# Performance work log

Measured on AMD Instinct MI355X. Metric: run time of the kernel, lower is better.

## Reference

```python
import jax, jax.numpy as jnp
import numpy as np

B, D, U1, U2 = 16384, 512, 512, 512
BN_EPS = 1e-3  # keras BatchNormalization default epsilon


def sparsemax(z):
    # z: [..., D]; standard sparsemax along last axis (Martins & Astudillo)
    d = z.shape[-1]
    z_sorted = -jnp.sort(-z, axis=-1)                      # descending
    z_cum = jnp.cumsum(z_sorted, axis=-1)
    k = jnp.arange(1, d + 1, dtype=z.dtype)
    support = (1.0 + k * z_sorted) > z_cum                 # [..., D] bool
    k_z = jnp.sum(support, axis=-1, keepdims=True)         # support size
    tau = (jnp.take_along_axis(z_cum, k_z.astype(jnp.int32) - 1, axis=-1) - 1.0) / k_z.astype(z.dtype)
    return jnp.maximum(z - tau, 0.0)


def setup_inputs() -> dict:
    key = jax.random.key(0)
    ks = jax.random.split(key, 8)
    x = jax.random.normal(ks[0], (B, D), dtype=jnp.float32)
    W1 = jax.random.normal(ks[1], (D, U1), dtype=jnp.float32) * 0.05
    b1 = jnp.zeros((U1,), jnp.float32)
    centers = jax.random.normal(ks[2], (U2, D), dtype=jnp.float32)      # paraboloid centers
    coefs = jax.random.normal(ks[3], (U2, D), dtype=jnp.float32) * 0.1  # paraboloid axis coefficients
    bn_gamma = jnp.ones((D,), jnp.float32)
    bn_beta = jnp.zeros((D,), jnp.float32)
    bn_mean = jnp.zeros((D,), jnp.float32)
    bn_var = jnp.ones((D,), jnp.float32)
    W_out = jax.random.normal(ks[4], (U1 + U2, D), dtype=jnp.float32) * 0.05
    b_out = jnp.zeros((D,), jnp.float32)
    w_add = jnp.array([0.5, 0.5], jnp.float32)  # WeightedAdd learnable scalars
    return {"x": x, "W1": W1, "b1": b1, "centers": centers, "coefs": coefs,
            "bn_gamma": bn_gamma, "bn_beta": bn_beta, "bn_mean": bn_mean, "bn_var": bn_var,
            "W_out": W_out, "b_out": b_out, "w_add": w_add}


def reference(x, W1, b1, centers, coefs, bn_gamma, bn_beta, bn_mean, bn_var, W_out, b_out, w_add):
    # Dense branch
    h1 = jax.nn.relu(x @ W1 + b1)                               # [B, U1]
    # BoundedParaboloids branch: BatchNorm (inference stats) then bounded paraboloids
    xb = (x - bn_mean) * jax.lax.rsqrt(bn_var + BN_EPS) * bn_gamma + bn_beta
    # q_j = sum_d (coefs[j,d] * (xb_d - centers[j,d]))^2, computed via GEMMs
    A = coefs * coefs                                            # [U2, D]
    q = (xb * xb) @ A.T - 2.0 * (xb @ (A * centers).T) + jnp.sum(A * centers * centers, axis=-1)
    h2 = jax.nn.relu(1.0 - q)                                    # [B, U2] bounded paraboloids
    # Output embedding: Dense(relu) on concat
    emb = jax.nn.relu(jnp.concatenate([h1, h2], axis=-1) @ W_out + b_out)  # [B, D]
    # WeightedAdd of (dropout-identity) inputs and embedding; dropout_rate=0 / inference
    pre = w_add[0] * x + w_add[1] * emb
    mask = sparsemax(pre)                                        # [B, D]
    return mask
```

## Files before the change

kernel.cpp:

```cpp
#include <hip/hip_runtime.h>
#include <math.h>

typedef float f4 __attribute__((ext_vector_type(4)));
typedef float f32x4 __attribute__((ext_vector_type(4)));
typedef __bf16 bf16x8 __attribute__((ext_vector_type(8)));
typedef unsigned short u16;
typedef u16 us8 __attribute__((ext_vector_type(8)));

__device__ __forceinline__ u16 f2bf(float f) {
  unsigned u = __builtin_bit_cast(unsigned, f);
  unsigned r = u + 0x7fffu + ((u >> 16) & 1u);
  return (u16)(r >> 16);
}
__device__ __forceinline__ float bf2f(u16 h) {
  unsigned u = ((unsigned)h) << 16;
  return __builtin_bit_cast(float, u);
}

__global__ __launch_bounds__(256) void prep_bn_kernel(
    const float* __restrict__ gamma, const float* __restrict__ beta,
    const float* __restrict__ mean, const float* __restrict__ var,
    float* __restrict__ scale, float* __restrict__ shift) {
  int d = blockIdx.x * blockDim.x + threadIdx.x;
  if (d < 512) {
    float s = rsqrtf(var[d] + 1e-3f) * gamma[d];
    scale[d] = s;
    shift[d] = beta[d] - mean[d] * s;
  }
}

__global__ __launch_bounds__(64) void prep_params_kernel(
    const float* __restrict__ coefs, const float* __restrict__ centers,
    u16* __restrict__ pth, float* __restrict__ cvec) {
  int j = blockIdx.x;
  int l = threadIdx.x;
  int d0 = l * 8;
  f4 c0 = *(const f4*)(coefs + (size_t)j * 512 + d0);
  f4 c1 = *(const f4*)(coefs + (size_t)j * 512 + d0 + 4);
  f4 e0 = *(const f4*)(centers + (size_t)j * 512 + d0);
  f4 e1 = *(const f4*)(centers + (size_t)j * 512 + d0 + 4);
  us8 pa, pb;
  float acc = 0.f;
#pragma unroll
  for (int e = 0; e < 8; ++e) {
    float cf = (e < 4) ? c0[e] : c1[e - 4];
    float ce = (e < 4) ? e0[e] : e1[e - 4];
    float a = cf * cf;
    pa[e] = f2bf(a);
    pb[e] = f2bf(-2.f * a * ce);
    acc = fmaf(a * ce, ce, acc);
  }
  *(us8*)(pth + (size_t)j * 1024 + d0) = pa;
  *(us8*)(pth + (size_t)j * 1024 + 512 + d0) = pb;
#pragma unroll
  for (int off = 32; off; off >>= 1) acc += __shfl_xor(acc, off);
  if (l == 0) cvec[j] = acc;
}

__global__ __launch_bounds__(256) void transpose_split_kernel(
    const float* __restrict__ in, u16* __restrict__ th, u16* __restrict__ tl,
    int K, int N) {
  __shared__ float t[32][33];
  int lx = threadIdx.x;
  int ly = threadIdx.y;
  int n0 = blockIdx.x * 32, k0 = blockIdx.y * 32;
#pragma unroll
  for (int i = 0; i < 4; ++i)
    t[ly + 8 * i][lx] = in[(size_t)(k0 + ly + 8 * i) * N + n0 + lx];
  __syncthreads();
#pragma unroll
  for (int i = 0; i < 4; ++i) {
    float v = t[lx][ly + 8 * i];
    u16 h = f2bf(v);
    th[(size_t)(n0 + ly + 8 * i) * K + k0 + lx] = h;
    if (tl) {
      u16 lo = f2bf(v - bf2f(h));
      tl[(size_t)(n0 + ly + 8 * i) * K + k0 + lx] = lo;
    }
  }
}

__global__ __launch_bounds__(256) void conv_x_kernel(
    const float* __restrict__ x, const float* __restrict__ scale,
    const float* __restrict__ shift, u16* __restrict__ xh,
    u16* __restrict__ xb) {
  int gid = blockIdx.x * 256 + threadIdx.x;
  int m = gid >> 6;
  int d0 = (gid & 63) * 8;
  f4 v0 = *(const f4*)(x + (size_t)m * 512 + d0);
  f4 v1 = *(const f4*)(x + (size_t)m * 512 + d0 + 4);
  f4 s0 = *(const f4*)(scale + d0);
  f4 s1 = *(const f4*)(scale + d0 + 4);
  f4 h0 = *(const f4*)(shift + d0);
  f4 h1 = *(const f4*)(shift + d0 + 4);
  us8 oh, ob;
#pragma unroll
  for (int e = 0; e < 8; ++e) {
    float xv = (e < 4) ? v0[e] : v1[e - 4];
    float sc = (e < 4) ? s0[e] : s1[e - 4];
    float sh = (e < 4) ? h0[e] : h1[e - 4];
    oh[e] = f2bf(xv);
    ob[e] = f2bf(fmaf(xv, sc, sh));
  }
  *(us8*)(xh + (size_t)m * 512 + d0) = oh;
  *(us8*)(xb + (size_t)m * 512 + d0) = ob;
}

__global__ __launch_bounds__(256, 4) void gemm_fused12(
    const u16* __restrict__ Xh, const u16* __restrict__ Xb,
    const u16* __restrict__ W1th, const u16* __restrict__ Pth,
    const float* __restrict__ b1, const float* __restrict__ cvec,
    u16* __restrict__ Hout) {
  extern __shared__ char smem[];
  char* sA = smem;
  char* sBh = smem + 16384;
  const int tid = threadIdx.x;
  const int l = tid & 63;
  const int w = tid >> 6;
  const int wm = w & 1, wn = w >> 1;
  const int lr = l & 15, lk = l >> 4;
  const int sx = lr & 7;
  const int bid = blockIdx.x;
  const int L = (bid & 7) * 128 + (bid >> 3);
  const int p = L >> 3;
  const int g = ((L >> 2) & 1) ^ 1;
  const int n = L & 3;
  const int m0 = p * 128, n0 = n * 128;
  const int Kg = g ? 1024 : 512;
  const u16* Bmat = g ? Pth : W1th;
  const u16* Amat = g ? Xb : Xh;
  const int srow = l >> 3;
  const int sslot = (l & 7) ^ srow;

  f32x4 acc[4][4];
#pragma unroll
  for (int i = 0; i < 4; ++i)
#pragma unroll
    for (int j = 0; j < 4; ++j) acc[i][j] = (f32x4){0.f, 0.f, 0.f, 0.f};

  for (int k0 = 0; k0 < Kg; k0 += 64) {
#pragma unroll
    for (int pp = 0; pp < 4; ++pp) {
      int c = pp * 4 + w;
      int row = c * 8 + srow;
      int loff = c * 1024;
      size_t gob = (size_t)(n0 + row) * Kg + k0 + sslot * 8;
      __builtin_amdgcn_global_load_lds(
          (const __attribute__((address_space(1))) void*)(Bmat + gob),
          (__attribute__((address_space(3))) void*)(sBh + loff), 16, 0, 0);
      if (g) {
        int kb = (k0 < 512) ? k0 : (k0 - 512);
        us8 v = *(const us8*)(Amat + (size_t)(m0 + row) * 512 + kb + sslot * 8);
        us8 o;
        if (k0 < 512) {
#pragma unroll
          for (int e = 0; e < 8; ++e) {
            float f = bf2f(v[e]);
            o[e] = f2bf(f * f);
          }
        } else {
          o = v;
        }
        *(us8*)(sA + loff + l * 16) = o;
      } else {
        size_t goa = (size_t)(m0 + row) * 512 + k0 + sslot * 8;
        __builtin_amdgcn_global_load_lds(
            (const __attribute__((address_space(1))) void*)(Amat + goa),
            (__attribute__((address_space(3))) void*)(sA + loff), 16, 0, 0);
      }
    }
    __syncthreads();
#pragma unroll
    for (int ks = 0; ks < 2; ++ks) {
      bf16x8 av[4], bv[4];
#pragma unroll
      for (int i = 0; i < 4; ++i)
        av[i] = *(const bf16x8*)(sA + (wm * 64 + i * 16 + lr) * 128 +
                                 (((ks * 4 + lk) ^ sx) * 16));
#pragma unroll
      for (int j = 0; j < 4; ++j)
        bv[j] = *(const bf16x8*)(sBh + (wn * 64 + j * 16 + lr) * 128 +
                                 (((ks * 4 + lk) ^ sx) * 16));
#pragma unroll
      for (int i = 0; i < 4; ++i)
#pragma unroll
        for (int j = 0; j < 4; ++j)
          acc[i][j] = __builtin_amdgcn_mfma_f32_16x16x32_bf16(av[i], bv[j],
                                                              acc[i][j], 0, 0, 0);
    }
    __syncthreads();
  }

  const int mwb = m0 + wm * 64;
  const int nwb = n0 + wn * 64;
  const float* bias = g ? cvec : b1;
#pragma unroll
  for (int j = 0; j < 4; ++j) {
    int nn = nwb + j * 16 + lr;
    float bv = bias[nn];
#pragma unroll
    for (int i = 0; i < 4; ++i) {
#pragma unroll
      for (int r = 0; r < 4; ++r) {
        int m = mwb + i * 16 + lk * 4 + r;
        float v = acc[i][j][r] + bv;
        v = g ? fmaxf(1.f - v, 0.f) : fmaxf(v, 0.f);
        Hout[(size_t)m * 1024 + g * 512 + nn] = f2bf(v);
      }
    }
  }
}

__global__ __launch_bounds__(256, 2) void gemm3(
    const u16* __restrict__ Ah, const u16* __restrict__ Bh,
    const float* __restrict__ bias, const float* __restrict__ xorig,
    const float* __restrict__ wadd, float* __restrict__ outp) {
  extern __shared__ char smem[];
  const int tid = threadIdx.x;
  const int l = tid & 63;
  const int w = tid >> 6;
  const int wm = w & 1, wn = w >> 1;
  const int lr = l & 15, lk = l >> 4;
  const int sx = lr & 7;
  const int bid = blockIdx.x;
  const int lin = (bid & 7) * 64 + (bid >> 3);
  const int m0 = (lin >> 2) * 128, n0 = (lin & 3) * 128;
  const int srow = l >> 3;
  const int sslot = (l & 7) ^ srow;

  f32x4 acc[4][4];
#pragma unroll
  for (int i = 0; i < 4; ++i)
#pragma unroll
    for (int j = 0; j < 4; ++j) acc[i][j] = (f32x4){0.f, 0.f, 0.f, 0.f};

#define G3_STAGE(buf, k0)                                                     \
  {                                                                           \
    char* dA = smem + (buf)*16384;                                            \
    char* dB = smem + 32768 + (buf)*16384;                                    \
    _Pragma("unroll") for (int pp = 0; pp < 4; ++pp) {                        \
      int c = pp * 4 + w;                                                     \
      int row = c * 8 + srow;                                                 \
      int loff = c * 1024;                                                    \
      size_t gob = (size_t)(n0 + row) * 1024 + (k0) + sslot * 8;              \
      size_t goa = (size_t)(m0 + row) * 1024 + (k0) + sslot * 8;              \
      __builtin_amdgcn_global_load_lds(                                       \
          (const __attribute__((address_space(1))) void*)(Bh + gob),          \
          (__attribute__((address_space(3))) void*)(dB + loff), 16, 0, 0);    \
      __builtin_amdgcn_global_load_lds(                                       \
          (const __attribute__((address_space(1))) void*)(Ah + goa),          \
          (__attribute__((address_space(3))) void*)(dA + loff), 16, 0, 0);    \
    }                                                                         \
  }

  G3_STAGE(0, 0);
  __syncthreads();
  for (int t = 0; t < 16; ++t) {
    if (t + 1 < 16) G3_STAGE((t + 1) & 1, (t + 1) * 64);
    const char* sA = smem + (t & 1) * 16384;
    const char* sB = smem + 32768 + (t & 1) * 16384;
#pragma unroll
    for (int ks = 0; ks < 2; ++ks) {
      bf16x8 av[4], bv[4];
#pragma unroll
      for (int i = 0; i < 4; ++i)
        av[i] = *(const bf16x8*)(sA + (wm * 64 + i * 16 + lr) * 128 +
                                 (((ks * 4 + lk) ^ sx) * 16));
#pragma unroll
      for (int j = 0; j < 4; ++j)
        bv[j] = *(const bf16x8*)(sB + (wn * 64 + j * 16 + lr) * 128 +
                                 (((ks * 4 + lk) ^ sx) * 16));
#pragma unroll
      for (int i = 0; i < 4; ++i)
#pragma unroll
        for (int j = 0; j < 4; ++j)
          acc[i][j] = __builtin_amdgcn_mfma_f32_16x16x32_bf16(av[i], bv[j],
                                                              acc[i][j], 0, 0, 0);
    }
    __syncthreads();
  }
#undef G3_STAGE

  const int mwb = m0 + wm * 64;
  const int nwb = n0 + wn * 64;
  float w0 = wadd[0], w1 = wadd[1];
#pragma unroll
  for (int j = 0; j < 4; ++j) {
    int n = nwb + j * 16 + lr;
    float bv = bias[n];
#pragma unroll
    for (int i = 0; i < 4; ++i) {
#pragma unroll
      for (int r = 0; r < 4; ++r) {
        int m = mwb + i * 16 + lk * 4 + r;
        float v = fmaxf(acc[i][j][r] + bv, 0.f);
        outp[(size_t)m * 512 + n] = fmaf(w1, v, w0 * xorig[(size_t)m * 512 + n]);
      }
    }
  }
}

__global__ __launch_bounds__(256) void sparsemax_kernel(float* __restrict__ out) {
  int row = blockIdx.x * 4 + (threadIdx.x >> 6);
  int lane = threadIdx.x & 63;
  float* rp = out + (size_t)row * 512;
  f4 z0 = *(const f4*)(rp + lane * 8);
  f4 z1 = *(const f4*)(rp + lane * 8 + 4);
  float z[8];
#pragma unroll
  for (int e = 0; e < 4; ++e) {
    z[e] = z0[e];
    z[4 + e] = z1[e];
  }
  float m = z[0];
#pragma unroll
  for (int i = 1; i < 8; ++i) m = fmaxf(m, z[i]);
#pragma unroll
  for (int off = 32; off; off >>= 1) m = fmaxf(m, __shfl_xor(m, off));
  float tau = m - 1.0f;
  for (int it = 0; it < 32; ++it) {
    float s = 0.f, k = 0.f;
#pragma unroll
    for (int i = 0; i < 8; ++i) {
      if (z[i] > tau) {
        s += z[i] - tau;
        k += 1.f;
      }
    }
#pragma unroll
    for (int off = 32; off; off >>= 1) {
      s += __shfl_xor(s, off);
      k += __shfl_xor(k, off);
    }
    if (k < 0.5f) break;
    float tn = tau + (s - 1.f) / k;
    if (tn == tau) break;
    tau = tn;
  }
  float s = 0.f, k = 0.f;
#pragma unroll
  for (int i = 0; i < 8; ++i)
    if (z[i] > tau) {
      s += z[i];
      k += 1.f;
    }
#pragma unroll
  for (int off = 32; off; off >>= 1) {
    s += __shfl_xor(s, off);
    k += __shfl_xor(k, off);
  }
  float tauf = (k >= 0.5f) ? (s - 1.f) / k : (m - 1.f);
  f4 o0, o1;
#pragma unroll
  for (int e = 0; e < 4; ++e) {
    o0[e] = fmaxf(z[e] - tauf, 0.f);
    o1[e] = fmaxf(z[4 + e] - tauf, 0.f);
  }
  *(f4*)(rp + lane * 8) = o0;
  *(f4*)(rp + lane * 8 + 4) = o1;
}

extern "C" void kernel_launch(void* const* d_in, const int* in_sizes, int n_in,
                              void* d_out, int out_size, void* d_ws,
                              size_t ws_size, hipStream_t stream) {
  const float* x = (const float*)d_in[0];
  const float* W1 = (const float*)d_in[1];
  const float* b1 = (const float*)d_in[2];
  const float* centers = (const float*)d_in[3];
  const float* coefs = (const float*)d_in[4];
  const float* gamma = (const float*)d_in[5];
  const float* beta = (const float*)d_in[6];
  const float* mean = (const float*)d_in[7];
  const float* var = (const float*)d_in[8];
  const float* W_out = (const float*)d_in[9];
  const float* b_out = (const float*)d_in[10];
  const float* wadd = (const float*)d_in[11];
  float* out = (float*)d_out;

  char* ws = (char*)d_ws;
  u16* Hh = (u16*)(ws);
  u16* Xh = (u16*)(ws + 33554432);
  u16* Xb = (u16*)(ws + 50331648);
  char* pool = ws + 67108864;
  u16* W1th = (u16*)(pool);
  u16* Pth = (u16*)(pool + 1048576);
  u16* Wth = (u16*)(pool);
  float* cvec = (float*)(ws + 69206016);
  float* scale = (float*)(ws + 69208064);
  float* shift = (float*)(ws + 69210112);

  prep_bn_kernel<<<2, 256, 0, stream>>>(gamma, beta, mean, var, scale, shift);
  prep_params_kernel<<<512, 64, 0, stream>>>(coefs, centers, Pth, cvec);
  transpose_split_kernel<<<dim3(16, 16), dim3(32, 8), 0, stream>>>(
      W1, W1th, nullptr, 512, 512);
  conv_x_kernel<<<4096, 256, 0, stream>>>(x, scale, shift, Xh, Xb);

  gemm_fused12<<<1024, 256, 32768, stream>>>(Xh, Xb, W1th, Pth, b1, cvec, Hh);

  transpose_split_kernel<<<dim3(16, 32), dim3(32, 8), 0, stream>>>(
      W_out, Wth, nullptr, 1024, 512);
  gemm3<<<512, 256, 65536, stream>>>(Hh, Wth, b_out, x, wadd, out);
  sparsemax_kernel<<<4096, 256, 0, stream>>>(out);
}
```

Before: 114.0 us.

## Double-buffer LDS tiles in fused GEMM and hoist W_out transpose

Restructures gemm_fused12 to double-buffer A and B tiles in 64KB of LDS, so the next K-tile is prefetched while MFMAs run on the current one. The squared-A path is staged through registers and written after compute. Launch bounds drop from 4 to 2 blocks per CU because of the larger LDS footprint. When the workspace is large enough, the W_out transpose moves before the GEMM into its own buffer, and the unused lo-split path of the transpose kernel is removed.

Result: faster. 111.2 us (-2.4%).

```diff
diff --git a/kernel.cpp b/kernel.cpp
--- a/kernel.cpp
+++ b/kernel.cpp
@@ -58,8 +58,7 @@
 }
 
 __global__ __launch_bounds__(256) void transpose_split_kernel(
-    const float* __restrict__ in, u16* __restrict__ th, u16* __restrict__ tl,
-    int K, int N) {
+    const float* __restrict__ in, u16* __restrict__ th, int K, int N) {
   __shared__ float t[32][33];
   int lx = threadIdx.x;
   int ly = threadIdx.y;
@@ -71,12 +70,7 @@
 #pragma unroll
   for (int i = 0; i < 4; ++i) {
     float v = t[lx][ly + 8 * i];
-    u16 h = f2bf(v);
-    th[(size_t)(n0 + ly + 8 * i) * K + k0 + lx] = h;
-    if (tl) {
-      u16 lo = f2bf(v - bf2f(h));
-      tl[(size_t)(n0 + ly + 8 * i) * K + k0 + lx] = lo;
-    }
+    th[(size_t)(n0 + ly + 8 * i) * K + k0 + lx] = f2bf(v);
   }
 }
 
@@ -106,14 +100,12 @@
   *(us8*)(xb + (size_t)m * 512 + d0) = ob;
 }
 
-__global__ __launch_bounds__(256, 4) void gemm_fused12(
+__global__ __launch_bounds__(256, 2) void gemm_fused12(
     const u16* __restrict__ Xh, const u16* __restrict__ Xb,
     const u16* __restrict__ W1th, const u16* __restrict__ Pth,
     const float* __restrict__ b1, const float* __restrict__ cvec,
     u16* __restrict__ Hout) {
   extern __shared__ char smem[];
-  char* sA = smem;
-  char* sBh = smem + 16384;
   const int tid = threadIdx.x;
   const int l = tid & 63;
   const int w = tid >> 6;
@@ -127,6 +119,7 @@
   const int n = L & 3;
   const int m0 = p * 128, n0 = n * 128;
   const int Kg = g ? 1024 : 512;
+  const int nt = g ? 16 : 8;
   const u16* Bmat = g ? Pth : W1th;
   const u16* Amat = g ? Xb : Xh;
   const int srow = l >> 3;
@@ -138,55 +131,120 @@
 #pragma unroll
     for (int j = 0; j < 4; ++j) acc[i][j] = (f32x4){0.f, 0.f, 0.f, 0.f};
 
-  for (int k0 = 0; k0 < Kg; k0 += 64) {
+  if (g) {
 #pragma unroll
     for (int pp = 0; pp < 4; ++pp) {
       int c = pp * 4 + w;
       int row = c * 8 + srow;
-      int loff = c * 1024;
-      size_t gob = (size_t)(n0 + row) * Kg + k0 + sslot * 8;
+      us8 v = *(const us8*)(Amat + (size_t)(m0 + row) * 512 + sslot * 8);
+      us8 o;
+#pragma unroll
+      for (int e = 0; e < 8; ++e) {
+        float f = bf2f(v[e]);
+        o[e] = f2bf(f * f);
+      }
+      *(us8*)(smem + c * 1024 + l * 16) = o;
+    }
+  } else {
+#pragma unroll
+    for (int pp = 0; pp < 4; ++pp) {
+      int c = pp * 4 + w;
+      int row = c * 8 + srow;
+      size_t goa = (size_t)(m0 + row) * 512 + sslot * 8;
       __builtin_amdgcn_global_load_lds(
-          (const __attribute__((address_space(1))) void*)(Bmat + gob),
-          (__attribute__((address_space(3))) void*)(sBh + loff), 16, 0, 0);
+          (const __attribute__((address_space(1))) void*)(Amat + goa),
+          (__attribute__((address_space(3))) void*)(smem + c * 1024), 16, 0, 0);
+    }
+  }
+#pragma unroll
+  for (int pp = 0; pp < 4; ++pp) {
+    int c = pp * 4 + w;
+    int row = c * 8 + srow;
+    size_t gob = (size_t)(n0 + row) * Kg + sslot * 8;
+    __builtin_amdgcn_global_load_lds(
+        (const __attribute__((address_space(1))) void*)(Bmat + gob),
+        (__attribute__((address_space(3))) void*)(smem + 32768 + c * 1024), 16,
+        0, 0);
+  }
+  __syncthreads();
+
+  for (int t = 0; t < nt; ++t) {
+    const int cur = t & 1, nxt = cur ^ 1;
+    const int k1 = (t + 1) * 64;
+    const bool more = (t + 1 < nt);
+    us8 areg[4];
+    if (more) {
       if (g) {
-        int kb = (k0 < 512) ? k0 : (k0 - 512);
-        us8 v = *(const us8*)(Amat + (size_t)(m0 + row) * 512 + kb + sslot * 8);
+        int kb = (k1 < 512) ? k1 : (k1 - 512);
+#pragma unroll
+        for (int pp = 0; pp < 4; ++pp) {
+          int c = pp * 4 + w;
+          int row = c * 8 + srow;
+          areg[pp] =
+              *(const us8*)(Amat + (size_t)(m0 + row) * 512 + kb + sslot * 8);
+        }
+      } else {
+#pragma unroll
+        for (int pp = 0; pp < 4; ++pp) {
+          int c = pp * 4 + w;
+          int row = c * 8 + srow;
+          size_t goa = (size_t)(m0 + row) * 512 + k1 + sslot * 8;
+          __builtin_amdgcn_global_load_lds(
+              (const __attribute__((address_space(1))) void*)(Amat + goa),
+              (__attribute__((address_space(3))) void*)(smem + nxt * 16384 +
+                                                        c * 1024),
+              16, 0, 0);
+        }
+      }
+#pragma unroll
+      for (int pp = 0; pp < 4; ++pp) {
+        int c = pp * 4 + w;
+        int row = c * 8 + srow;
+        size_t gob = (size_t)(n0 + row) * Kg + k1 + sslot * 8;
+        __builtin_amdgcn_global_load_lds(
+            (const __attribute__((address_space(1))) void*)(Bmat + gob),
+            (__attribute__((address_space(3))) void*)(smem + 32768 +
+                                                      nxt * 16384 + c * 1024),
+            16, 0, 0);
+      }
+    }
+    const char* sA = smem + cur * 16384;
+    const char* sB = smem + 32768 + cur * 16384;
+#pragma unroll
+    for (int ks = 0; ks < 2; ++ks) {
+      bf16x8 av[4], bv[4];
+#pragma unroll
+      for (int i = 0; i < 4; ++i)
+        av[i] = *(const bf16x8*)(sA + (wm * 64 + i * 16 + lr) * 128 +
+                                 (((ks * 4 + lk) ^ sx) * 16));
+#pragma unroll
+      for (int j = 0; j < 4; ++j)
+        bv[j] = *(const bf16x8*)(sB + (wn * 64 + j * 16 + lr) * 128 +
+                                 (((ks * 4 + lk) ^ sx) * 16));
+#pragma unroll
+      for (int i = 0; i < 4; ++i)
+#pragma unroll
+        for (int j = 0; j < 4; ++j)
+          acc[i][j] = __builtin_amdgcn_mfma_f32_16x16x32_bf16(av[i], bv[j],
+                                                              acc[i][j], 0, 0, 0);
+    }
+    if (more && g) {
+      const bool sq = (k1 < 512);
+#pragma unroll
+      for (int pp = 0; pp < 4; ++pp) {
+        int c = pp * 4 + w;
         us8 o;
-        if (k0 < 512) {
+        if (sq) {
 #pragma unroll
           for (int e = 0; e < 8; ++e) {
-            float f = bf2f(v[e]);
+            float f = bf2f(areg[pp][e]);
             o[e] = f2bf(f * f);
           }
         } else {
-          o = v;
+          o = areg[pp];
         }
-        *(us8*)(sA + loff + l * 16) = o;
-      } else {
-        size_t goa = (size_t)(m0 + row) * 512 + k0 + sslot * 8;
-        __builtin_amdgcn_global_load_lds(
-            (const __attribute__((address_space(1))) void*)(Amat + goa),
-            (__attribute__((address_space(3))) void*)(sA + loff), 16, 0, 0);
-      }
-    }
-    __syncthreads();
-#pragma unroll
-    for (int ks = 0; ks < 2; ++ks) {
-      bf16x8 av[4], bv[4];
-#pragma unroll
-      for (int i = 0; i < 4; ++i)
-        av[i] = *(const bf16x8*)(sA + (wm * 64 + i * 16 + lr) * 128 +
-                                 (((ks * 4 + lk) ^ sx) * 16));
-#pragma unroll
-      for (int j = 0; j < 4; ++j)
-        bv[j] = *(const bf16x8*)(sBh + (wn * 64 + j * 16 + lr) * 128 +
-                                 (((ks * 4 + lk) ^ sx) * 16));
-#pragma unroll
-      for (int i = 0; i < 4; ++i)
-#pragma unroll
-        for (int j = 0; j < 4; ++j)
-          acc[i][j] = __builtin_amdgcn_mfma_f32_16x16x32_bf16(av[i], bv[j],
-                                                              acc[i][j], 0, 0, 0);
+        *(us8*)(smem + nxt * 16384 + c * 1024 + l * 16) = o;
+      }
     }
     __syncthreads();
   }
@@ -384,21 +442,28 @@
   char* pool = ws + 67108864;
   u16* W1th = (u16*)(pool);
   u16* Pth = (u16*)(pool + 1048576);
-  u16* Wth = (u16*)(pool);
   float* cvec = (float*)(ws + 69206016);
   float* scale = (float*)(ws + 69208064);
   float* shift = (float*)(ws + 69210112);
+  const bool bigws = (ws_size >= (size_t)70260736);
+  u16* Wth = bigws ? (u16*)(ws + 69212160) : (u16*)(pool);
 
   prep_bn_kernel<<<2, 256, 0, stream>>>(gamma, beta, mean, var, scale, shift);
   prep_params_kernel<<<512, 64, 0, stream>>>(coefs, centers, Pth, cvec);
-  transpose_split_kernel<<<dim3(16, 16), dim3(32, 8), 0, stream>>>(
-      W1, W1th, nullptr, 512, 512);
+  transpose_split_kernel<<<dim3(16, 16), dim3(32, 8), 0, stream>>>(W1, W1th,
+                                                                   512, 512);
+  if (bigws) {
+    transpose_split_kernel<<<dim3(16, 32), dim3(32, 8), 0, stream>>>(
+        W_out, Wth, 1024, 512);
+  }
   conv_x_kernel<<<4096, 256, 0, stream>>>(x, scale, shift, Xh, Xb);
 
-  gemm_fused12<<<1024, 256, 32768, stream>>>(Xh, Xb, W1th, Pth, b1, cvec, Hh);
-
-  transpose_split_kernel<<<dim3(16, 32), dim3(32, 8), 0, stream>>>(
-      W_out, Wth, nullptr, 1024, 512);
+  gemm_fused12<<<1024, 256, 65536, stream>>>(Xh, Xb, W1th, Pth, b1, cvec, Hh);
+
+  if (!bigws) {
+    transpose_split_kernel<<<dim3(16, 32), dim3(32, 8), 0, stream>>>(
+        W_out, Wth, 1024, 512);
+  }
   gemm3<<<512, 256, 65536, stream>>>(Hh, Wth, b_out, x, wadd, out);
   sparsemax_kernel<<<4096, 256, 0, stream>>>(out);
 }
```

## Double-buffer fused GEMM12 LDS loads and precompute squared BN input

Applied to the files above, without the earlier changes.

The first fused GEMM now double-buffers its LDS tiles, issuing async global-to-LDS loads for the next K-tile while MFMAs run on the current one. The squared batch-normalized input is precomputed in the conversion kernel into the output buffer, so both A operands use direct LDS loads instead of register squaring. The W_out transpose is moved to a separate workspace region when space allows, removing a dependency. LDS doubles to 64KB and occupancy is lowered to 2 blocks per CU, and an extra 16MB bf16 tensor is written and read.

After: 107.7 us. 5.5% less time.

```diff
diff --git a/kernel.cpp b/kernel.cpp
--- a/kernel.cpp
+++ b/kernel.cpp
@@ -58,8 +58,7 @@
 }
 
 __global__ __launch_bounds__(256) void transpose_split_kernel(
-    const float* __restrict__ in, u16* __restrict__ th, u16* __restrict__ tl,
-    int K, int N) {
+    const float* __restrict__ in, u16* __restrict__ th, int K, int N) {
   __shared__ float t[32][33];
   int lx = threadIdx.x;
   int ly = threadIdx.y;
@@ -71,19 +70,14 @@
 #pragma unroll
   for (int i = 0; i < 4; ++i) {
     float v = t[lx][ly + 8 * i];
-    u16 h = f2bf(v);
-    th[(size_t)(n0 + ly + 8 * i) * K + k0 + lx] = h;
-    if (tl) {
-      u16 lo = f2bf(v - bf2f(h));
-      tl[(size_t)(n0 + ly + 8 * i) * K + k0 + lx] = lo;
-    }
+    th[(size_t)(n0 + ly + 8 * i) * K + k0 + lx] = f2bf(v);
   }
 }
 
 __global__ __launch_bounds__(256) void conv_x_kernel(
     const float* __restrict__ x, const float* __restrict__ scale,
     const float* __restrict__ shift, u16* __restrict__ xh,
-    u16* __restrict__ xb) {
+    u16* __restrict__ xb, u16* __restrict__ xsq) {
   int gid = blockIdx.x * 256 + threadIdx.x;
   int m = gid >> 6;
   int d0 = (gid & 63) * 8;
@@ -93,27 +87,28 @@
   f4 s1 = *(const f4*)(scale + d0 + 4);
   f4 h0 = *(const f4*)(shift + d0);
   f4 h1 = *(const f4*)(shift + d0 + 4);
-  us8 oh, ob;
+  us8 oh, ob, oq;
 #pragma unroll
   for (int e = 0; e < 8; ++e) {
     float xv = (e < 4) ? v0[e] : v1[e - 4];
     float sc = (e < 4) ? s0[e] : s1[e - 4];
     float sh = (e < 4) ? h0[e] : h1[e - 4];
     oh[e] = f2bf(xv);
-    ob[e] = f2bf(fmaf(xv, sc, sh));
+    float xbf = fmaf(xv, sc, sh);
+    ob[e] = f2bf(xbf);
+    oq[e] = f2bf(xbf * xbf);
   }
   *(us8*)(xh + (size_t)m * 512 + d0) = oh;
   *(us8*)(xb + (size_t)m * 512 + d0) = ob;
-}
-
-__global__ __launch_bounds__(256, 4) void gemm_fused12(
+  *(us8*)(xsq + (size_t)m * 512 + d0) = oq;
+}
+
+__global__ __launch_bounds__(256, 2) void gemm_fused12(
     const u16* __restrict__ Xh, const u16* __restrict__ Xb,
-    const u16* __restrict__ W1th, const u16* __restrict__ Pth,
-    const float* __restrict__ b1, const float* __restrict__ cvec,
-    u16* __restrict__ Hout) {
+    const u16* __restrict__ Xsq, const u16* __restrict__ W1th,
+    const u16* __restrict__ Pth, const float* __restrict__ b1,
+    const float* __restrict__ cvec, u16* __restrict__ Hout) {
   extern __shared__ char smem[];
-  char* sA = smem;
-  char* sBh = smem + 16384;
   const int tid = threadIdx.x;
   const int l = tid & 63;
   const int w = tid >> 6;
@@ -127,8 +122,8 @@
   const int n = L & 3;
   const int m0 = p * 128, n0 = n * 128;
   const int Kg = g ? 1024 : 512;
+  const int nt = g ? 16 : 8;
   const u16* Bmat = g ? Pth : W1th;
-  const u16* Amat = g ? Xb : Xh;
   const int srow = l >> 3;
   const int sslot = (l & 7) ^ srow;
 
@@ -138,38 +133,33 @@
 #pragma unroll
     for (int j = 0; j < 4; ++j) acc[i][j] = (f32x4){0.f, 0.f, 0.f, 0.f};
 
-  for (int k0 = 0; k0 < Kg; k0 += 64) {
-#pragma unroll
-    for (int pp = 0; pp < 4; ++pp) {
-      int c = pp * 4 + w;
-      int row = c * 8 + srow;
-      int loff = c * 1024;
-      size_t gob = (size_t)(n0 + row) * Kg + k0 + sslot * 8;
-      __builtin_amdgcn_global_load_lds(
-          (const __attribute__((address_space(1))) void*)(Bmat + gob),
-          (__attribute__((address_space(3))) void*)(sBh + loff), 16, 0, 0);
-      if (g) {
-        int kb = (k0 < 512) ? k0 : (k0 - 512);
-        us8 v = *(const us8*)(Amat + (size_t)(m0 + row) * 512 + kb + sslot * 8);
-        us8 o;
-        if (k0 < 512) {
-#pragma unroll
-          for (int e = 0; e < 8; ++e) {
-            float f = bf2f(v[e]);
-            o[e] = f2bf(f * f);
-          }
-        } else {
-          o = v;
-        }
-        *(us8*)(sA + loff + l * 16) = o;
-      } else {
-        size_t goa = (size_t)(m0 + row) * 512 + k0 + sslot * 8;
-        __builtin_amdgcn_global_load_lds(
-            (const __attribute__((address_space(1))) void*)(Amat + goa),
-            (__attribute__((address_space(3))) void*)(sA + loff), 16, 0, 0);
-      }
-    }
-    __syncthreads();
+#define F12_STAGE(buf, k0)                                                    \
+  {                                                                           \
+    const u16* Asrc = g ? (((k0) < 512) ? Xsq : Xb) : Xh;                     \
+    const int kb = (k0)&511;                                                  \
+    char* dA = smem + (buf)*16384;                                            \
+    char* dB = smem + 32768 + (buf)*16384;                                    \
+    _Pragma("unroll") for (int pp = 0; pp < 4; ++pp) {                        \
+      int c = pp * 4 + w;                                                     \
+      int row = c * 8 + srow;                                                 \
+      int loff = c * 1024;                                                    \
+      size_t goa = (size_t)(m0 + row) * 512 + kb + sslot * 8;                 \
+      size_t gob = (size_t)(n0 + row) * Kg + (k0) + sslot * 8;                \
+      __builtin_amdgcn_global_load_lds(                                       \
+          (const __attribute__((address_space(1))) void*)(Asrc + goa),        \
+          (__attribute__((address_space(3))) void*)(dA + loff), 16, 0, 0);    \
+      __builtin_amdgcn_global_load_lds(                                       \
+          (const __attribute__((address_space(1))) void*)(Bmat + gob),        \
+          (__attribute__((address_space(3))) void*)(dB + loff), 16, 0, 0);    \
+    }                                                                         \
+  }
+
+  F12_STAGE(0, 0);
+  __syncthreads();
+  for (int t = 0; t < nt; ++t) {
+    if (t + 1 < nt) F12_STAGE((t + 1) & 1, (t + 1) * 64);
+    const char* sA = smem + (t & 1) * 16384;
+    const char* sB = smem + 32768 + (t & 1) * 16384;
 #pragma unroll
     for (int ks = 0; ks < 2; ++ks) {
       bf16x8 av[4], bv[4];
@@ -179,7 +169,7 @@
                                  (((ks * 4 + lk) ^ sx) * 16));
 #pragma unroll
       for (int j = 0; j < 4; ++j)
-        bv[j] = *(const bf16x8*)(sBh + (wn * 64 + j * 16 + lr) * 128 +
+        bv[j] = *(const bf16x8*)(sB + (wn * 64 + j * 16 + lr) * 128 +
                                  (((ks * 4 + lk) ^ sx) * 16));
 #pragma unroll
       for (int i = 0; i < 4; ++i)
@@ -190,6 +180,7 @@
     }
     __syncthreads();
   }
+#undef F12_STAGE
 
   const int mwb = m0 + wm * 64;
   const int nwb = n0 + wn * 64;
@@ -384,21 +375,30 @@
   char* pool = ws + 67108864;
   u16* W1th = (u16*)(pool);
   u16* Pth = (u16*)(pool + 1048576);
-  u16* Wth = (u16*)(pool);
   float* cvec = (float*)(ws + 69206016);
   float* scale = (float*)(ws + 69208064);
   float* shift = (float*)(ws + 69210112);
+  u16* Xsq = (u16*)d_out;
+  const bool bigws = (ws_size >= (size_t)70260736);
+  u16* Wth = bigws ? (u16*)(ws + 69212160) : (u16*)(pool);
 
   prep_bn_kernel<<<2, 256, 0, stream>>>(gamma, beta, mean, var, scale, shift);
   prep_params_kernel<<<512, 64, 0, stream>>>(coefs, centers, Pth, cvec);
-  transpose_split_kernel<<<dim3(16, 16), dim3(32, 8), 0, stream>>>(
-      W1, W1th, nullptr, 512, 512);
-  conv_x_kernel<<<4096, 256, 0, stream>>>(x, scale, shift, Xh, Xb);
-
-  gemm_fused12<<<1024, 256, 32768, stream>>>(Xh, Xb, W1th, Pth, b1, cvec, Hh);
-
-  transpose_split_kernel<<<dim3(16, 32), dim3(32, 8), 0, stream>>>(
-      W_out, Wth, nullptr, 1024, 512);
+  transpose_split_kernel<<<dim3(16, 16), dim3(32, 8), 0, stream>>>(W1, W1th,
+                                                                   512, 512);
+  if (bigws) {
+    transpose_split_kernel<<<dim3(16, 32), dim3(32, 8), 0, stream>>>(
+        W_out, Wth, 1024, 512);
+  }
+  conv_x_kernel<<<4096, 256, 0, stream>>>(x, scale, shift, Xh, Xb, Xsq);
+
+  gemm_fused12<<<1024, 256, 65536, stream>>>(Xh, Xb, Xsq, W1th, Pth, b1, cvec,
+                                             Hh);
+
+  if (!bigws) {
+    transpose_split_kernel<<<dim3(16, 32), dim3(32, 8), 0, stream>>>(
+        W_out, Wth, 1024, 512);
+  }
   gemm3<<<512, 256, 65536, stream>>>(Hh, Wth, b_out, x, wadd, out);
   sparsemax_kernel<<<4096, 256, 0, stream>>>(out);
 }
```
